# Kernel optimization log

Hardware: AMD Instinct MI355X
Metric: run time of the kernel (lower is better)

Reference implementation:

```python
import jax, jax.numpy as jnp
import numpy as np


def setup_inputs() -> dict:
    key = jax.random.key(0)
    ks = jax.random.split(key, 7)
    N, C, sy, sx = 1024, 384, 7, 7
    Dm, Dc = 64, 64
    Dg = C + Dm + Dc  # 512, must match f_t_global
    return {
        "f_t_global": jax.random.normal(ks[0], (N, Dg), dtype=jnp.float32),
        "x_t_local": jax.random.normal(ks[1], (N, C, sy, sx), dtype=jnp.float32),
        "x_t_prev_local": jax.random.normal(ks[2], (N, C, sy, sx), dtype=jnp.float32),
        "m_t": jax.random.normal(ks[3], (N, Dm), dtype=jnp.float32),
        "m_t_prev": jax.random.normal(ks[4], (N, Dm), dtype=jnp.float32),
        "c_t": jax.random.normal(ks[5], (N, Dc), dtype=jnp.float32),
        "c_t_prev": jax.random.normal(ks[6], (N, Dc), dtype=jnp.float32),
    }


def _join(loc, m, c):
    # loc: [S, N, C]; m: [N, Dm]; c: [N, Dc] -> [S, N, C+Dm+Dc]
    S, N, _ = loc.shape
    mc = jnp.concatenate([m, c], axis=-1)  # [N, Dm+Dc]
    mc = jnp.broadcast_to(mc[None], (S, N, mc.shape[-1]))
    return jnp.concatenate([loc, mc], axis=-1)


def _mean_ce_diag(logits):
    # logits: [S, N, N]; labels = arange(N) for every s -> mean over s of CE
    logp = jax.nn.log_softmax(logits, axis=-1)
    diag = jnp.diagonal(logp, axis1=1, axis2=2)  # [S, N]
    return -jnp.mean(diag)  # mean over N (per-step CE) and over S (the /(sx*sy))


def reference(f_t_global, x_t_local, x_t_prev_local, m_t, m_t_prev, c_t, c_t_prev):
    N, C, sy, sx = x_t_prev_local.shape
    S = sy * sx
    # [N,C,sy,sx] -> [S,N,C] (spatial locations batched)
    prev = x_t_prev_local.reshape(N, C, S).transpose(2, 0, 1)
    cur = x_t_local.reshape(N, C, S).transpose(2, 0, 1)
    pos = _join(prev, m_t_prev, c_t_prev)   # [S, N, D]
    # loss1: global features vs per-location previous positives
    logits1 = jnp.einsum('id,sjd->sij', f_t_global, pos)  # [S, N, N]
    loss1 = _mean_ce_diag(logits1)
    # loss2: per-location current predictions vs previous positives
    pred2 = _join(cur, m_t, c_t)            # [S, N, D]
    logits2 = jnp.einsum('sid,sjd->sij', pred2, pos)
    loss2 = _mean_ce_diag(logits2)
    loss = loss1 + loss2
    return (loss, x_t_prev_local, x_t_local)
```

## Files before the change

### kernel.cpp

```cpp
#include <hip/hip_runtime.h>
#include <hip/hip_bf16.h>

typedef __attribute__((ext_vector_type(8))) __bf16 bf16x8;
typedef __attribute__((ext_vector_type(4))) float  f32x4;

#define SDIM 49
#define NDIM 1024
#define CDIM 384
#define DDIM 512
#define DMC  64
#define SCALE (1.0f/(SDIM*NDIM))
#define SLOT 65536

__device__ __forceinline__ void gload16(const void* g, void* l) {
    __builtin_amdgcn_global_load_lds((const __attribute__((address_space(1))) void*)g,
                                     (__attribute__((address_space(3))) void*)l, 16, 0, 0);
}

__global__ __launch_bounds__(512) void pack_copy_kernel(
    const float* __restrict__ xloc, const float* __restrict__ mv,
    const float* __restrict__ cv,   __hip_bfloat16* __restrict__ dst,
    float* __restrict__ cpy)
{
    const int j = blockIdx.x;
    const int d = threadIdx.x;
    float vals[SDIM];
    if (d < CDIM) {
        const float* p = xloc + ((size_t)j * CDIM + d) * SDIM;
        #pragma unroll
        for (int s = 0; s < SDIM; ++s) vals[s] = p[s];
        float* dcp = cpy + ((size_t)j * CDIM + d) * SDIM;
        #pragma unroll
        for (int s = 0; s < SDIM; ++s) dcp[s] = vals[s];
    } else if (d < CDIM + DMC) {
        float v = mv[j * DMC + (d - CDIM)];
        #pragma unroll
        for (int s = 0; s < SDIM; ++s) vals[s] = v;
    } else {
        float v = cv[j * DMC + (d - CDIM - DMC)];
        #pragma unroll
        for (int s = 0; s < SDIM; ++s) vals[s] = v;
    }
    #pragma unroll
    for (int s = 0; s < SDIM; ++s)
        dst[((size_t)s * NDIM + j) * DDIM + d] = __float2bfloat16(vals[s]);
}

__global__ void fpack_kernel(const float* __restrict__ f,
                             __hip_bfloat16* __restrict__ dst, int n)
{
    int i = blockIdx.x * blockDim.x + threadIdx.x;
    if (i < n) dst[i] = __float2bfloat16(f[i]);
}

__global__ __launch_bounds__(512, 2) void loss_kernel(
    const __hip_bfloat16* __restrict__ Fm,
    const __hip_bfloat16* __restrict__ Km,
    const __hip_bfloat16* __restrict__ Qm,
    float2* __restrict__ part,
    float* __restrict__ out)
{
    extern __shared__ __attribute__((aligned(16))) char sm[];

    const int bid = blockIdx.x;
    const int xcd = bid & 7;
    const int jj  = bid >> 3;
    const int g0  = 196 * xcd;
    const int gend = g0 + 196;

    const int tid  = threadIdx.x;
    const int lane = tid & 63;
    const int w    = tid >> 6;
    const int l15  = lane & 15;
    const int l4   = lane >> 4;
    const int wk   = w >> 2;
    const int wq   = w & 3;

    const int trow = tid >> 3;
    const int scol = (((tid & 7) ^ ((tid >> 3) & 7)) << 4);

    const unsigned xo   = (unsigned)((l15 & 7) << 4);
    const unsigned arow = (unsigned)((wk * 128 + l15) * 128);
    const unsigned brow = 32768u + (unsigned)((wq * 64 + l15) * 128);

    auto APtr = [&](int gg) -> const char* {
        const int s = gg >> 5, kb = (gg >> 3) & 3;
        return (const char*)Km + ((size_t)s * NDIM + (size_t)kb * 256) * 1024;
    };
    auto BPtr = [&](int gg) -> const char* {
        const int s = gg >> 5, qb = gg & 7;
        return (qb < 4)
            ? ((const char*)Fm + (size_t)qb * 256 * 1024)
            : ((const char*)Qm + ((size_t)s * NDIM + (size_t)(qb - 4) * 256) * 1024);
    };
    auto stage4 = [&](const char* A, const char* B, int ko, char* slot, int h) {
        #pragma unroll
        for (int c = 2 * h; c < 2 * h + 2; ++c) {
            gload16(A + (size_t)(c * 64 + trow) * 1024 + ko + scol,
                    slot + c * 8192 + tid * 16);
            gload16(B + (size_t)(c * 64 + trow) * 1024 + ko + scol,
                    slot + 32768 + c * 8192 + tid * 16);
        }
    };

    f32x4 acc[8][4];
    bf16x8 afr[4][2], bfr[4][2];

    #define READ_A(H) do {                                                    \
        _Pragma("unroll")                                                     \
        for (int a = 0; a < 4; ++a)                                           \
            _Pragma("unroll")                                                 \
            for (int kc = 0; kc < 2; ++kc)                                    \
                afr[a][kc] = *(const bf16x8*)(sb_ + arow + (H) * 8192u        \
                    + a * 2048u + (((unsigned)(kc * 64 + l4 * 16)) ^ xo));    \
    } while (0)

    #define READ_B(H) do {                                                    \
        _Pragma("unroll")                                                     \
        for (int b = 0; b < 2; ++b)                                           \
            _Pragma("unroll")                                                 \
            for (int kc = 0; kc < 2; ++kc)                                    \
                bfr[(H)*2 + b][kc] = *(const bf16x8*)(sb_ + brow              \
                    + ((H)*2 + b) * 2048u                                     \
                    + (((unsigned)(kc * 64 + l4 * 16)) ^ xo));                \
    } while (0)

    #define MFMA_Q(AH, BH) do {                                               \
        _Pragma("unroll")                                                     \
        for (int a = 0; a < 4; ++a)                                           \
            _Pragma("unroll")                                                 \
            for (int b = 0; b < 2; ++b)                                       \
                _Pragma("unroll")                                             \
                for (int kc = 0; kc < 2; ++kc)                                \
                    acc[(AH)*4 + a][(BH)*2 + b] =                             \
                        __builtin_amdgcn_mfma_f32_16x16x32_bf16(              \
                            afr[a][kc], bfr[(BH)*2 + b][kc],                  \
                            acc[(AH)*4 + a][(BH)*2 + b], 0, 0, 0);            \
    } while (0)

    {
        const char* A0 = APtr(g0 + jj);
        const char* B0 = BPtr(g0 + jj);
        stage4(A0, B0, 0, sm, 0);
        stage4(A0, B0, 0, sm, 1);
    }

    for (int g = g0 + jj; g < gend; g += 32) {
        const char* Ag = APtr(g);
        const char* Bg = BPtr(g);
        const bool hasNext = (g + 32) < gend;
        const char* An = hasNext ? APtr(g + 32) : Ag;
        const char* Bn = hasNext ? BPtr(g + 32) : Bg;

        #pragma unroll
        for (int a = 0; a < 8; ++a)
            #pragma unroll
            for (int b = 0; b < 4; ++b) acc[a][b] = f32x4{0.f, 0.f, 0.f, 0.f};

        #pragma unroll
        for (int t = 0; t < 8; ++t) {
            const char* sb_ = sm + (size_t)(t & 1) * SLOT;
            char* ns_ = sm + (size_t)((t + 1) & 1) * SLOT;
            const bool pf = (t < 7) || hasNext;
            const char* sA = (t < 7) ? Ag : An;
            const char* sB = (t < 7) ? Bg : Bn;
            const int ko = (t < 7) ? (t + 1) * 128 : 0;

            asm volatile("s_waitcnt vmcnt(0)" ::: "memory");
            __builtin_amdgcn_s_barrier();
            if (pf) stage4(sA, sB, ko, ns_, 0);
            READ_A(0); READ_B(0);
            __builtin_amdgcn_s_barrier();
            asm volatile("s_waitcnt lgkmcnt(0)" ::: "memory");
            __builtin_amdgcn_s_setprio(1); MFMA_Q(0, 0); __builtin_amdgcn_s_setprio(0);
            __builtin_amdgcn_s_barrier();
            if (pf) stage4(sA, sB, ko, ns_, 1);
            READ_B(1);
            __builtin_amdgcn_s_barrier();
            asm volatile("s_waitcnt lgkmcnt(0)" ::: "memory");
            __builtin_amdgcn_s_setprio(1); MFMA_Q(0, 1); __builtin_amdgcn_s_setprio(0);
            __builtin_amdgcn_s_barrier();
            READ_A(1);
            __builtin_amdgcn_s_barrier();
            asm volatile("s_waitcnt lgkmcnt(0)" ::: "memory");
            __builtin_amdgcn_s_setprio(1); MFMA_Q(1, 0); __builtin_amdgcn_s_setprio(0);
            __builtin_amdgcn_s_barrier();
            __builtin_amdgcn_s_setprio(1); MFMA_Q(1, 1); __builtin_amdgcn_s_setprio(0);
        }

        const int s  = g >> 5;
        const int kb = (g >> 3) & 3;
        const int qb = g & 7;

        float q_m[4], q_s[4];
        #pragma unroll
        for (int b = 0; b < 4; ++b) {
            float m = -3.0e38f;
            #pragma unroll
            for (int a = 0; a < 8; ++a)
                #pragma unroll
                for (int r = 0; r < 4; ++r) m = fmaxf(m, acc[a][b][r]);
            float ss = 0.0f;
            #pragma unroll
            for (int a = 0; a < 8; ++a)
                #pragma unroll
                for (int r = 0; r < 4; ++r) ss += __expf(acc[a][b][r] - m);
            #pragma unroll
            for (int off = 16; off <= 32; off <<= 1) {
                float mo = __shfl_xor(m, off, 64);
                float so = __shfl_xor(ss, off, 64);
                float nm = fmaxf(m, mo);
                ss = ss * __expf(m - nm) + so * __expf(mo - nm);
                m = nm;
            }
            q_m[b] = m; q_s[b] = ss;
        }
        if (lane < 16) {
            const size_t rowb = (size_t)s * 2048 + (size_t)qb * 256 + wq * 64 + lane;
            #pragma unroll
            for (int b = 0; b < 4; ++b)
                part[(rowb + b * 16) * 8 + kb * 2 + wk] = make_float2(q_m[b], q_s[b]);
        }

        if (kb == (qb & 3) && (wq >> 1) == wk) {
            float d = 0.0f;
            const bool lok = (((lane >> 2) & 3) == l4);
            if (wq & 1) {
                #pragma unroll
                for (int b = 0; b < 4; ++b)
                    #pragma unroll
                    for (int r = 0; r < 4; ++r)
                        if (lok && r == (lane & 3)) d += acc[4 + b][b][r];
            } else {
                #pragma unroll
                for (int b = 0; b < 4; ++b)
                    #pragma unroll
                    for (int r = 0; r < 4; ++r)
                        if (lok && r == (lane & 3)) d += acc[b][b][r];
            }
            #pragma unroll
            for (int off = 1; off < 64; off <<= 1) d += __shfl_xor(d, off, 64);
            if (lane == 0) atomicAdd(out, -d * SCALE);
        }
    }
    #undef READ_A
    #undef READ_B
    #undef MFMA_Q
}

__global__ __launch_bounds__(256) void reduce_kernel(
    const float2* __restrict__ part, float* __restrict__ out)
{
    const int row = blockIdx.x * 256 + threadIdx.x;
    const float2* p = part + (size_t)row * 8;
    float m = -3.0e38f;
    float2 q[8];
    #pragma unroll
    for (int i = 0; i < 8; ++i) { q[i] = p[i]; m = fmaxf(m, q[i].x); }
    float ssum = 0.0f;
    #pragma unroll
    for (int i = 0; i < 8; ++i) ssum += q[i].y * __expf(q[i].x - m);
    float v = m + __logf(ssum);
    #pragma unroll
    for (int off = 1; off < 64; off <<= 1) v += __shfl_xor(v, off, 64);
    __shared__ float red[4];
    const int lane = threadIdx.x & 63, w = threadIdx.x >> 6;
    if (lane == 0) red[w] = v;
    __syncthreads();
    if (threadIdx.x == 0)
        atomicAdd(out, (red[0] + red[1] + red[2] + red[3]) * SCALE);
}

extern "C" void kernel_launch(void* const* d_in, const int* in_sizes, int n_in,
                              void* d_out, int out_size, void* d_ws, size_t ws_size,
                              hipStream_t stream)
{
    (void)in_sizes; (void)n_in; (void)out_size; (void)ws_size;
    const float* f  = (const float*)d_in[0];
    const float* x  = (const float*)d_in[1];
    const float* xp = (const float*)d_in[2];
    const float* mt = (const float*)d_in[3];
    const float* mp = (const float*)d_in[4];
    const float* ct = (const float*)d_in[5];
    const float* cp = (const float*)d_in[6];
    float* out = (float*)d_out;

    char* ws = (char*)d_ws;
    const size_t packBytes = (size_t)SDIM * NDIM * DDIM * 2;
    __hip_bfloat16* Km = (__hip_bfloat16*)ws;
    __hip_bfloat16* Qm = (__hip_bfloat16*)(ws + packBytes);
    __hip_bfloat16* Fm = (__hip_bfloat16*)(ws + 2 * packBytes);
    float2* part = (float2*)(ws + 2 * packBytes + (size_t)NDIM * DDIM * 2);

    hipMemsetAsync(out, 0, sizeof(float), stream);

    const int sz = NDIM * CDIM * SDIM;
    pack_copy_kernel<<<NDIM, 512, 0, stream>>>(xp, mp, cp, Km, out + 1);
    pack_copy_kernel<<<NDIM, 512, 0, stream>>>(x,  mt, ct, Qm, out + 1 + sz);
    fpack_kernel<<<(NDIM * DDIM + 255) / 256, 256, 0, stream>>>(f, Fm, NDIM * DDIM);

    loss_kernel<<<256, 512, 2 * SLOT, stream>>>(Fm, Km, Qm, part, out);
    reduce_kernel<<<392, 256, 0, stream>>>(part, out);
}
```

Baseline: 260.0 us.

## Simplify GEMM K-step schedule to one barrier with full-tile prefetch

Replaces the quadrant-split inner step, which used several s_barriers, split half-tile prefetches and separate A/B fragment reads, with a simpler schedule. Each K-step now does one __syncthreads, issues the whole next-tile global-to-LDS prefetch at once, then does two rounds of reading 8 A and 4 B fragments followed by 32 MFMAs. The goal is to cut barrier and waitcnt overhead and let the compiler schedule LDS reads and MFMAs more freely. The cost is less explicit interleaving of LDS reads with MFMA work, and correctness now depends on __syncthreads draining the async LDS loads.

Result: faster. 241.7 us (-7.0%).

```diff
diff --git a/kernel.cpp b/kernel.cpp
--- a/kernel.cpp
+++ b/kernel.cpp
@@ -83,19 +83,19 @@
     const unsigned arow = (unsigned)((wk * 128 + l15) * 128);
     const unsigned brow = 32768u + (unsigned)((wq * 64 + l15) * 128);
 
-    auto APtr = [&](int gg) -> const char* {
-        const int s = gg >> 5, kb = (gg >> 3) & 3;
+    auto APtr = [&](int g) -> const char* {
+        const int s = g >> 5, kb = (g >> 3) & 3;
         return (const char*)Km + ((size_t)s * NDIM + (size_t)kb * 256) * 1024;
     };
-    auto BPtr = [&](int gg) -> const char* {
-        const int s = gg >> 5, qb = gg & 7;
+    auto BPtr = [&](int g) -> const char* {
+        const int s = g >> 5, qb = g & 7;
         return (qb < 4)
             ? ((const char*)Fm + (size_t)qb * 256 * 1024)
             : ((const char*)Qm + ((size_t)s * NDIM + (size_t)(qb - 4) * 256) * 1024);
     };
-    auto stage4 = [&](const char* A, const char* B, int ko, char* slot, int h) {
-        #pragma unroll
-        for (int c = 2 * h; c < 2 * h + 2; ++c) {
+    auto stage8 = [&](const char* A, const char* B, int ko, char* slot) {
+        #pragma unroll
+        for (int c = 0; c < 4; ++c) {
             gload16(A + (size_t)(c * 64 + trow) * 1024 + ko + scol,
                     slot + c * 8192 + tid * 16);
             gload16(B + (size_t)(c * 64 + trow) * 1024 + ko + scol,
@@ -104,46 +104,28 @@
     };
 
     f32x4 acc[8][4];
-    bf16x8 afr[4][2], bfr[4][2];
-
-    #define READ_A(H) do {                                                    \
+    bf16x8 afr[8], bfr[4];
+
+    #define READ12(KC) do {                                                   \
+        const unsigned co = ((unsigned)((KC) * 64 + l4 * 16)) ^ xo;           \
         _Pragma("unroll")                                                     \
-        for (int a = 0; a < 4; ++a)                                           \
+        for (int a = 0; a < 8; ++a)                                           \
+            afr[a] = *(const bf16x8*)(sb_ + arow + a * 2048u + co);           \
+        _Pragma("unroll")                                                     \
+        for (int b = 0; b < 4; ++b)                                           \
+            bfr[b] = *(const bf16x8*)(sb_ + brow + b * 2048u + co);           \
+    } while (0)
+
+    #define MFMA32() do {                                                     \
+        _Pragma("unroll")                                                     \
+        for (int a = 0; a < 8; ++a)                                           \
             _Pragma("unroll")                                                 \
-            for (int kc = 0; kc < 2; ++kc)                                    \
-                afr[a][kc] = *(const bf16x8*)(sb_ + arow + (H) * 8192u        \
-                    + a * 2048u + (((unsigned)(kc * 64 + l4 * 16)) ^ xo));    \
+            for (int b = 0; b < 4; ++b)                                       \
+                acc[a][b] = __builtin_amdgcn_mfma_f32_16x16x32_bf16(          \
+                    afr[a], bfr[b], acc[a][b], 0, 0, 0);                      \
     } while (0)
 
-    #define READ_B(H) do {                                                    \
-        _Pragma("unroll")                                                     \
-        for (int b = 0; b < 2; ++b)                                           \
-            _Pragma("unroll")                                                 \
-            for (int kc = 0; kc < 2; ++kc)                                    \
-                bfr[(H)*2 + b][kc] = *(const bf16x8*)(sb_ + brow              \
-                    + ((H)*2 + b) * 2048u                                     \
-                    + (((unsigned)(kc * 64 + l4 * 16)) ^ xo));                \
-    } while (0)
-
-    #define MFMA_Q(AH, BH) do {                                               \
-        _Pragma("unroll")                                                     \
-        for (int a = 0; a < 4; ++a)                                           \
-            _Pragma("unroll")                                                 \
-            for (int b = 0; b < 2; ++b)                                       \
-                _Pragma("unroll")                                             \
-                for (int kc = 0; kc < 2; ++kc)                                \
-                    acc[(AH)*4 + a][(BH)*2 + b] =                             \
-                        __builtin_amdgcn_mfma_f32_16x16x32_bf16(              \
-                            afr[a][kc], bfr[(BH)*2 + b][kc],                  \
-                            acc[(AH)*4 + a][(BH)*2 + b], 0, 0, 0);            \
-    } while (0)
-
-    {
-        const char* A0 = APtr(g0 + jj);
-        const char* B0 = BPtr(g0 + jj);
-        stage4(A0, B0, 0, sm, 0);
-        stage4(A0, B0, 0, sm, 1);
-    }
+    stage8(APtr(g0 + jj), BPtr(g0 + jj), 0, sm);
 
     for (int g = g0 + jj; g < gend; g += 32) {
         const char* Ag = APtr(g);
@@ -161,31 +143,20 @@
         for (int t = 0; t < 8; ++t) {
             const char* sb_ = sm + (size_t)(t & 1) * SLOT;
             char* ns_ = sm + (size_t)((t + 1) & 1) * SLOT;
-            const bool pf = (t < 7) || hasNext;
-            const char* sA = (t < 7) ? Ag : An;
-            const char* sB = (t < 7) ? Bg : Bn;
-            const int ko = (t < 7) ? (t + 1) * 128 : 0;
-
-            asm volatile("s_waitcnt vmcnt(0)" ::: "memory");
-            __builtin_amdgcn_s_barrier();
-            if (pf) stage4(sA, sB, ko, ns_, 0);
-            READ_A(0); READ_B(0);
-            __builtin_amdgcn_s_barrier();
-            asm volatile("s_waitcnt lgkmcnt(0)" ::: "memory");
-            __builtin_amdgcn_s_setprio(1); MFMA_Q(0, 0); __builtin_amdgcn_s_setprio(0);
-            __builtin_amdgcn_s_barrier();
-            if (pf) stage4(sA, sB, ko, ns_, 1);
-            READ_B(1);
-            __builtin_amdgcn_s_barrier();
-            asm volatile("s_waitcnt lgkmcnt(0)" ::: "memory");
-            __builtin_amdgcn_s_setprio(1); MFMA_Q(0, 1); __builtin_amdgcn_s_setprio(0);
-            __builtin_amdgcn_s_barrier();
-            READ_A(1);
-            __builtin_amdgcn_s_barrier();
-            asm volatile("s_waitcnt lgkmcnt(0)" ::: "memory");
-            __builtin_amdgcn_s_setprio(1); MFMA_Q(1, 0); __builtin_amdgcn_s_setprio(0);
-            __builtin_amdgcn_s_barrier();
-            __builtin_amdgcn_s_setprio(1); MFMA_Q(1, 1); __builtin_amdgcn_s_setprio(0);
+
+            __syncthreads();
+
+            if ((t < 7) || hasNext) {
+                const char* sA = (t < 7) ? Ag : An;
+                const char* sB = (t < 7) ? Bg : Bn;
+                stage8(sA, sB, (t < 7) ? (t + 1) * 128 : 0, ns_);
+            }
+            __builtin_amdgcn_sched_barrier(0);
+
+            READ12(0);
+            __builtin_amdgcn_s_setprio(1); MFMA32(); __builtin_amdgcn_s_setprio(0);
+            READ12(1);
+            __builtin_amdgcn_s_setprio(1); MFMA32(); __builtin_amdgcn_s_setprio(0);
         }
 
         const int s  = g >> 5;
@@ -243,9 +214,8 @@
             if (lane == 0) atomicAdd(out, -d * SCALE);
         }
     }
-    #undef READ_A
-    #undef READ_B
-    #undef MFMA_Q
+    #undef READ12
+    #undef MFMA32
 }
 
 __global__ __launch_bounds__(256) void reduce_kernel(
```
